# Performance work log

Hardware: AMD Instinct MI355X
Metric: run time of the kernel (lower is better)

The kernel has to match this reference:

```python
import jax, jax.numpy as jnp
import numpy as np

B, N, DIM, H, DH = 8, 1024, 512, 8, 64
INNER = H * DH  # 512
G = DH // 4     # SE(3) groups of size 4 per head


def setup_inputs() -> dict:
    key = jax.random.key(0)
    ks = jax.random.split(key, 6)
    x = jax.random.normal(ks[0], (B, N, DIM), jnp.float32)
    rotations = jax.random.normal(ks[1], (B, N, 3, 3), jnp.float32)
    translations = jax.random.normal(ks[2], (B, N, 3), jnp.float32)
    # JaxLinear init: trunc-normal std = 1/sqrt(fan_in), zero bias
    w_qkv = jax.random.normal(ks[3], (DIM, 3 * INNER), jnp.float32) * (1.0 / np.sqrt(DIM))
    b_qkv = jnp.zeros((3 * INNER,), jnp.float32)
    w_out = jax.random.normal(ks[4], (INNER, DIM), jnp.float32) * (1.0 / np.sqrt(INNER))
    b_out = jnp.zeros((DIM,), jnp.float32)
    return {"x": x, "rotations": rotations, "translations": translations,
            "w_qkv": w_qkv, "b_qkv": b_qkv, "w_out": w_out, "b_out": b_out}


def _apply_pose(P, t, transpose):
    # P: [B,N,4,4]; t: [B,H,N,DH] -> reshape to groups of 4 and rotate each group
    tg = t.reshape(B, H, N, G, 4)
    sub = 'bnji,bhncj->bhnci' if transpose else 'bnij,bhncj->bhnci'
    return jnp.einsum(sub, P, tg).reshape(B, H, N, DH)


def reference(x, rotations, translations, w_qkv, b_qkv, w_out, b_out):
    scale = DH ** -0.5
    qkv = x @ w_qkv + b_qkv                      # [B,N,3*INNER]
    q, k, v = jnp.split(qkv, 3, axis=-1)
    to_heads = lambda t: t.reshape(B, N, H, DH).transpose(0, 2, 1, 3)  # b n (h d) -> b h n d
    q, k, v = to_heads(q), to_heads(k), to_heads(v)

    # SE(3) pose matrices
    eye4 = jnp.eye(4, dtype=x.dtype)
    Rt = jnp.swapaxes(rotations, -1, -2)
    t_inv = -jnp.einsum('bnij,bnj->bni', Rt, translations)
    P_qinv = (jnp.broadcast_to(eye4, (B, N, 4, 4))
              .at[..., :3, :3].set(Rt)
              .at[..., :3, 3].set(t_inv))       # inverted query poses
    P_kv = (jnp.broadcast_to(eye4, (B, N, 4, 4))
            .at[..., :3, :3].set(rotations)
            .at[..., :3, 3].set(translations))  # key/value poses

    # per-token rotation of q/k/v (q uses P_qinv^T per original einsum)
    q = _apply_pose(P_qinv, q, transpose=True)
    k = _apply_pose(P_kv, k, transpose=False)
    v = _apply_pose(P_kv, v, transpose=False)   # v_transform=True

    attn = jax.nn.softmax(jnp.einsum('bhqd,bhkd->bhqk', q, k) * scale, axis=-1)
    out = jnp.einsum('bhqk,bhkd->bhqd', attn, v)
    out = _apply_pose(P_qinv, out, transpose=False)  # inverse transform on output

    out = out.transpose(0, 2, 1, 3).reshape(B, N, INNER)  # b h n d -> b n (h d)
    return out @ w_out + b_out
```

## Files before the change

kernel.cpp:

```cpp
#include <hip/hip_runtime.h>
#include <math.h>

#define BSZ   8
#define NSEQ  1024
#define DIM   512
#define NH    8
#define DH    64
#define INNER 512
#define NTOK  (BSZ*NSEQ)
#define QKVN  (3*INNER)

typedef __bf16 bf16x8 __attribute__((ext_vector_type(8)));
typedef float  f32x4  __attribute__((ext_vector_type(4)));

#define QSCL (0.125f * 1.44269504088896f)

static __device__ __forceinline__ ushort f2bf(float f) {
    union { float f; unsigned u; } v; v.f = f;
    unsigned r = (v.u + 0x7FFFu + ((v.u >> 16) & 1u)) >> 16;
    return (ushort)r;
}
static __device__ __forceinline__ float bf2f(ushort u) {
    union { unsigned u; float f; } v; v.u = ((unsigned)u) << 16;
    return v.f;
}
static __device__ __forceinline__ void split2(float x, ushort& h, ushort& l) {
    h = f2bf(x);
    l = f2bf(x - bf2f(h));
}
static __device__ __forceinline__ void async16(const void* g, void* l) {
    __builtin_amdgcn_global_load_lds(
        (const __attribute__((address_space(1))) unsigned int*)g,
        (__attribute__((address_space(3))) unsigned int*)l, 16, 0, 0);
}

__global__ __launch_bounds__(256) void split_cvt_kernel(
    const float* __restrict__ in, ushort* __restrict__ oh, ushort* __restrict__ ol)
{
    const int i = blockIdx.x * 256 + threadIdx.x;
    float4 v = ((const float4*)in)[i];
    ushort4 h, l;
    split2(v.x, h.x, l.x); split2(v.y, h.y, l.y);
    split2(v.z, h.z, l.z); split2(v.w, h.w, l.w);
    ((ushort4*)oh)[i] = h;
    ((ushort4*)ol)[i] = l;
}

__global__ __launch_bounds__(256) void tconv_split_kernel(
    const float* __restrict__ in, ushort* __restrict__ outh,
    ushort* __restrict__ outl, int K, int F)
{
    __shared__ float tile[32][33];
    const int bx = blockIdx.x;
    const int by = blockIdx.y;
    const int lx = threadIdx.x & 31, ly = threadIdx.x >> 5;
#pragma unroll
    for (int u = 0; u < 4; u++) {
        const int k = by*32 + ly + u*8;
        tile[ly + u*8][lx] = in[(size_t)k*F + bx*32 + lx];
    }
    __syncthreads();
#pragma unroll
    for (int u = 0; u < 4; u++) {
        const int f = bx*32 + ly + u*8;
        ushort h, l;
        split2(tile[lx][ly + u*8], h, l);
        outh[(size_t)f*K + by*32 + lx] = h;
        outl[(size_t)f*K + by*32 + lx] = l;
    }
}

__global__ __launch_bounds__(256) void vtrans_kernel(
    const ushort* __restrict__ vb, ushort* __restrict__ vt)
{
    __shared__ ushort tile[64][72];
    const int nt = blockIdx.x;
    const int bh = blockIdx.y;
    const int tid = threadIdx.x;
    const ushort* src = vb + (size_t)bh*NSEQ*DH + (size_t)nt*64*DH;
    ushort* dst = vt + (size_t)bh*DH*NSEQ + nt*64;

#pragma unroll
    for (int u = 0; u < 2; u++) {
        const int idx = tid + u*256;
        const int row = idx >> 3;
        const int col = (idx & 7) * 8;
        *(uint4*)&tile[row][col] = *(const uint4*)(src + row*DH + col);
    }
    __syncthreads();
#pragma unroll
    for (int u = 0; u < 2; u++) {
        const int idx = tid + u*256;
        const int d   = idx >> 3;
        const int n0  = (idx & 7) * 8;
        ushort tmp[8];
#pragma unroll
        for (int i = 0; i < 8; i++) tmp[i] = tile[n0+i][d];
        *(uint4*)&dst[(size_t)d*NSEQ + n0] = *(uint4*)tmp;
    }
}

__global__ __launch_bounds__(256) void qkv_gemm_split(
    const ushort* __restrict__ Agh, const ushort* __restrict__ Agl,
    const ushort* __restrict__ Bgh, const ushort* __restrict__ Bgl,
    const float* __restrict__ bias, const float* __restrict__ rot,
    const float* __restrict__ trans,
    ushort* __restrict__ qb, ushort* __restrict__ kb, ushort* __restrict__ vb)
{
    extern __shared__ __align__(16) char smem[];

    const int tid  = threadIdx.x;
    const int lane = tid & 63;
    const int w    = tid >> 6;
    const int c    = lane & 15;
    const int quad = lane >> 4;
    const int wr   = w >> 1, wc = w & 1;
    const int tn   = blockIdx.x;
    const int tf   = blockIdx.y;

    f32x4 acc[4][4] = {};

    const ushort* wp = (w == 0) ? Agh : (w == 1) ? Agl : (w == 2) ? Bgh : Bgl;
    const ushort* wbase = wp + (size_t)((w < 2 ? tf : tn)*128 + c)*DIM + quad*8;

    auto stage = [&](int k0, int buf) {
#pragma unroll
        for (int g = 0; g < 8; g++)
            async16(wbase + (size_t)g*16*DIM + k0,
                    smem + buf*32768 + (w*8 + g)*1024);
    };

    stage(0, 0);

    for (int ch = 0; ch < 16; ch++) {
        const int cur = ch & 1, nxt = cur ^ 1;
        if (ch < 15) {
            stage((ch+1)*32, nxt);
            __asm__ volatile("s_waitcnt vmcnt(8)\n\ts_barrier" ::: "memory");
        } else {
            __asm__ volatile("s_waitcnt vmcnt(0)\n\ts_barrier" ::: "memory");
        }

        const char* B = smem + cur*32768;
        bf16x8 fah[4], fal[4], fbh[4], fbl[4];
#pragma unroll
        for (int i = 0; i < 4; i++) {
            fah[i] = *(const bf16x8*)(B + ( 0 + wr*4 + i)*1024 + lane*16);
            fal[i] = *(const bf16x8*)(B + ( 8 + wr*4 + i)*1024 + lane*16);
        }
#pragma unroll
        for (int j = 0; j < 4; j++) {
            fbh[j] = *(const bf16x8*)(B + (16 + wc*4 + j)*1024 + lane*16);
            fbl[j] = *(const bf16x8*)(B + (24 + wc*4 + j)*1024 + lane*16);
        }
#pragma unroll
        for (int i = 0; i < 4; i++)
#pragma unroll
            for (int j = 0; j < 4; j++) {
                acc[i][j] = __builtin_amdgcn_mfma_f32_16x16x32_bf16(
                    fah[i], fbh[j], acc[i][j], 0, 0, 0);
                acc[i][j] = __builtin_amdgcn_mfma_f32_16x16x32_bf16(
                    fah[i], fbl[j], acc[i][j], 0, 0, 0);
                acc[i][j] = __builtin_amdgcn_mfma_f32_16x16x32_bf16(
                    fal[i], fbh[j], acc[i][j], 0, 0, 0);
            }
        __asm__ volatile("s_waitcnt lgkmcnt(0)\n\ts_barrier" ::: "memory");
    }

    const int sec = tf >> 2;
    ushort* dstbuf = (sec == 0) ? qb : ((sec == 1) ? kb : vb);

#pragma unroll
    for (int j = 0; j < 4; j++) {
        const int tc = tn*128 + wc*64 + j*16 + c;
        const int bb = tc >> 10, n = tc & 1023;
        const float* R = rot   + (size_t)(bb*NSEQ + n)*9;
        const float* T = trans + (size_t)(bb*NSEQ + n)*3;
        const float R0=R[0],R1=R[1],R2=R[2],R3=R[3],R4=R[4],R5=R[5],R6=R[6],R7=R[7],R8=R[8];
        const float T0=T[0],T1=T[1],T2=T[2];
        float ti0 = 0.f, ti1 = 0.f, ti2 = 0.f;
        if (sec == 0) {
            ti0 = -(R0*T0 + R3*T1 + R6*T2);
            ti1 = -(R1*T0 + R4*T1 + R7*T2);
            ti2 = -(R2*T0 + R5*T1 + R8*T2);
        }
#pragma unroll
        for (int i = 0; i < 4; i++) {
            const int fr = tf*128 + wr*64 + i*16 + quad*4;
            const int fl = fr & 511;
            const int h  = fl >> 6, d = fl & 63;
            float4 bv = *(const float4*)(bias + fr);
            const float g0 = acc[i][j][0] + bv.x;
            const float g1 = acc[i][j][1] + bv.y;
            const float g2 = acc[i][j][2] + bv.z;
            const float g3 = acc[i][j][3] + bv.w;
            float o0, o1, o2, o3;
            if (sec == 0) {
                o0 = (R0*g0 + R1*g1 + R2*g2) * QSCL;
                o1 = (R3*g0 + R4*g1 + R5*g2) * QSCL;
                o2 = (R6*g0 + R7*g1 + R8*g2) * QSCL;
                o3 = (ti0*g0 + ti1*g1 + ti2*g2 + g3) * QSCL;
            } else {
                o0 = R0*g0 + R1*g1 + R2*g2 + T0*g3;
                o1 = R3*g0 + R4*g1 + R5*g2 + T1*g3;
                o2 = R6*g0 + R7*g1 + R8*g2 + T2*g3;
                o3 = g3;
            }
            ushort4 ov = { f2bf(o0), f2bf(o1), f2bf(o2), f2bf(o3) };
            *(ushort4*)(dstbuf + ((size_t)((bb*NH + h)*NSEQ + n))*DH + d) = ov;
        }
    }
}

__global__ __launch_bounds__(256) void attn_mfma_kernel(
    const ushort* __restrict__ qb, const ushort* __restrict__ kb,
    const ushort* __restrict__ vt, const float* __restrict__ rot,
    const float* __restrict__ trans,
    ushort* __restrict__ omh, ushort* __restrict__ oml)
{
    __shared__ __align__(16) char smem[51200];

    const int tid  = threadIdx.x;
    const int lane = tid & 63;
    const int w    = tid >> 6;
    const int c    = lane & 15;
    const int quad = lane >> 4;

    const int qt = blockIdx.x;
    const int bh = blockIdx.y;
    const int bb = bh >> 3, h = bh & 7;

    const ushort* Q = qb + (size_t)bh * NSEQ * DH;
    const ushort* K = kb + (size_t)bh * NSEQ * DH;
    const ushort* V = vt + (size_t)bh * DH * NSEQ;

    bf16x8 qf[2][2];
#pragma unroll
    for (int m = 0; m < 2; m++) {
        const ushort* qrow = Q + (size_t)(qt*128 + w*32 + m*16 + c)*DH + quad*8;
        qf[m][0] = *(const bf16x8*)(qrow);
        qf[m][1] = *(const bf16x8*)(qrow + 32);
    }

    f32x4 Oacc[2][4] = {};
    float lsum[2][4] = {};

    auto stage = [&](int kt, int buf) {
#pragma unroll
        for (int u = 0; u < 2; u++) {
            const int seg = w + u*4;
            const int nt = seg >> 1, hh = seg & 1;
            const ushort* g = K + (size_t)(kt*64 + nt*16 + c)*DH + hh*32 + quad*8;
            async16(g, smem + buf*16384 + seg*1024);
        }
#pragma unroll
        for (int u = 0; u < 2; u++) {
            const int s2 = w + u*4;
            const int nt = s2 >> 1, kc = s2 & 1;
            const ushort* g = V + (size_t)(nt*16 + c)*NSEQ + kt*64 + kc*32 + quad*8;
            async16(g, smem + buf*16384 + 8192 + s2*1024);
        }
    };

    stage(0, 0);
    __syncthreads();

    for (int kt = 0; kt < 16; kt++) {
        const int cur = kt & 1, nxt = cur ^ 1;
        if (kt < 15) stage(kt+1, nxt);

        const char* Kb = smem + cur*16384;
        const char* Vb = smem + cur*16384 + 8192;

        f32x4 s[2][4];
#pragma unroll
        for (int nt = 0; nt < 4; nt++) {
            bf16x8 k0 = *(const bf16x8*)(Kb + (nt*2+0)*1024 + lane*16);
            bf16x8 k1 = *(const bf16x8*)(Kb + (nt*2+1)*1024 + lane*16);
#pragma unroll
            for (int m = 0; m < 2; m++) {
                f32x4 a = {0.f, 0.f, 0.f, 0.f};
                a = __builtin_amdgcn_mfma_f32_16x16x32_bf16(qf[m][0], k0, a, 0, 0, 0);
                a = __builtin_amdgcn_mfma_f32_16x16x32_bf16(qf[m][1], k1, a, 0, 0, 0);
                s[m][nt] = a;
            }
        }

#pragma unroll
        for (int m = 0; m < 2; m++) {
            ushort (*Psw)[72] = (ushort (*)[72])(smem + 32768 + (w*2+m)*2304);
#pragma unroll
            for (int nt = 0; nt < 4; nt++)
#pragma unroll
                for (int r = 0; r < 4; r++) {
                    const float p = exp2f(s[m][nt][r]);
                    lsum[m][r] += p;
                    Psw[quad*4 + r][nt*16 + c] = (ushort)__builtin_bit_cast(
                        unsigned short, (__bf16)p);
                }
        }
        __asm__ volatile("s_waitcnt lgkmcnt(0)" ::: "memory");

#pragma unroll
        for (int kc = 0; kc < 2; kc++) {
            bf16x8 vfr[4];
#pragma unroll
            for (int nt = 0; nt < 4; nt++)
                vfr[nt] = *(const bf16x8*)(Vb + (nt*2+kc)*1024 + lane*16);
#pragma unroll
            for (int m = 0; m < 2; m++) {
                ushort (*Psw)[72] = (ushort (*)[72])(smem + 32768 + (w*2+m)*2304);
                bf16x8 a = *(const bf16x8*)&Psw[c][kc*32 + quad*8];
#pragma unroll
                for (int nt = 0; nt < 4; nt++)
                    Oacc[m][nt] = __builtin_amdgcn_mfma_f32_16x16x32_bf16(
                        a, vfr[nt], Oacc[m][nt], 0, 0, 0);
            }
        }
        __syncthreads();
    }

#pragma unroll
    for (int mk = 1; mk < 16; mk <<= 1)
#pragma unroll
        for (int m = 0; m < 2; m++)
#pragma unroll
            for (int r = 0; r < 4; r++)
                lsum[m][r] += __shfl_xor(lsum[m][r], mk);

    float (*Osh)[68] = (float (*)[68])smem;
    {
        float inv[2][4];
#pragma unroll
        for (int m = 0; m < 2; m++)
#pragma unroll
            for (int r = 0; r < 4; r++) inv[m][r] = 1.f / lsum[m][r];
#pragma unroll
        for (int m = 0; m < 2; m++)
#pragma unroll
            for (int nt = 0; nt < 4; nt++)
#pragma unroll
                for (int r = 0; r < 4; r++)
                    Osh[w*32 + m*16 + quad*4 + r][nt*16 + c] =
                        Oacc[m][nt][r] * inv[m][r];
    }
    __syncthreads();

#pragma unroll
    for (int u = 0; u < 8; u++) {
        const int t   = tid + u*256;
        const int row = t >> 4;
        const int g   = t & 15;
        const int n   = qt*128 + row;
        const float o0 = Osh[row][g*4+0], o1 = Osh[row][g*4+1];
        const float o2 = Osh[row][g*4+2], o3 = Osh[row][g*4+3];
        const float* R = rot   + (size_t)(bb*NSEQ + n)*9;
        const float* T = trans + (size_t)(bb*NSEQ + n)*3;
        const float ti0 = -(R[0]*T[0] + R[3]*T[1] + R[6]*T[2]);
        const float ti1 = -(R[1]*T[0] + R[4]*T[1] + R[7]*T[2]);
        const float ti2 = -(R[2]*T[0] + R[5]*T[1] + R[8]*T[2]);
        const float p0 = R[0]*o0 + R[3]*o1 + R[6]*o2 + ti0*o3;
        const float p1 = R[1]*o0 + R[4]*o1 + R[7]*o2 + ti1*o3;
        const float p2 = R[2]*o0 + R[5]*o1 + R[8]*o2 + ti2*o3;
        const float p3 = o3;
        ushort4 hv, lv;
        split2(p0, hv.x, lv.x); split2(p1, hv.y, lv.y);
        split2(p2, hv.z, lv.z); split2(p3, hv.w, lv.w);
        const size_t idx = (size_t)(bb*NSEQ + n)*INNER + h*DH + g*4;
        *(ushort4*)(omh + idx) = hv;
        *(ushort4*)(oml + idx) = lv;
    }
}

__global__ __launch_bounds__(256) void out_gemm_split(
    const ushort* __restrict__ Agh, const ushort* __restrict__ Agl,
    const ushort* __restrict__ Bgh, const ushort* __restrict__ Bgl,
    const float* __restrict__ bias, float* __restrict__ out)
{
    extern __shared__ __align__(16) char smem[];

    const int tid  = threadIdx.x;
    const int lane = tid & 63;
    const int w    = tid >> 6;
    const int c    = lane & 15;
    const int quad = lane >> 4;
    const int wr   = w >> 1, wc = w & 1;
    const int tn   = blockIdx.x;
    const int tf   = blockIdx.y;

    f32x4 acc[4][4] = {};

    const ushort* wp = (w == 0) ? Agh : (w == 1) ? Agl : (w == 2) ? Bgh : Bgl;
    const ushort* wbase = wp + (size_t)((w < 2 ? tf : tn)*128 + c)*INNER + quad*8;

    auto stage = [&](int k0, int buf) {
#pragma unroll
        for (int g = 0; g < 8; g++)
            async16(wbase + (size_t)g*16*INNER + k0,
                    smem + buf*32768 + (w*8 + g)*1024);
    };

    stage(0, 0);

    for (int ch = 0; ch < 16; ch++) {
        const int cur = ch & 1, nxt = cur ^ 1;
        if (ch < 15) {
            stage((ch+1)*32, nxt);
            __asm__ volatile("s_waitcnt vmcnt(8)\n\ts_barrier" ::: "memory");
        } else {
            __asm__ volatile("s_waitcnt vmcnt(0)\n\ts_barrier" ::: "memory");
        }

        const char* B = smem + cur*32768;
        bf16x8 fah[4], fal[4], fbh[4], fbl[4];
#pragma unroll
        for (int i = 0; i < 4; i++) {
            fah[i] = *(const bf16x8*)(B + ( 0 + wr*4 + i)*1024 + lane*16);
            fal[i] = *(const bf16x8*)(B + ( 8 + wr*4 + i)*1024 + lane*16);
        }
#pragma unroll
        for (int j = 0; j < 4; j++) {
            fbh[j] = *(const bf16x8*)(B + (16 + wc*4 + j)*1024 + lane*16);
            fbl[j] = *(const bf16x8*)(B + (24 + wc*4 + j)*1024 + lane*16);
        }
#pragma unroll
        for (int i = 0; i < 4; i++)
#pragma unroll
            for (int j = 0; j < 4; j++) {
                acc[i][j] = __builtin_amdgcn_mfma_f32_16x16x32_bf16(
                    fah[i], fbh[j], acc[i][j], 0, 0, 0);
                acc[i][j] = __builtin_amdgcn_mfma_f32_16x16x32_bf16(
                    fah[i], fbl[j], acc[i][j], 0, 0, 0);
                acc[i][j] = __builtin_amdgcn_mfma_f32_16x16x32_bf16(
                    fal[i], fbh[j], acc[i][j], 0, 0, 0);
            }
        __asm__ volatile("s_waitcnt lgkmcnt(0)\n\ts_barrier" ::: "memory");
    }

#pragma unroll
    for (int j = 0; j < 4; j++) {
        const int tc = tn*128 + wc*64 + j*16 + c;
#pragma unroll
        for (int i = 0; i < 4; i++) {
            const int fr = tf*128 + wr*64 + i*16 + quad*4;
            float4 bv = *(const float4*)(bias + fr);
            float4 ov = { acc[i][j][0] + bv.x, acc[i][j][1] + bv.y,
                          acc[i][j][2] + bv.z, acc[i][j][3] + bv.w };
            *(float4*)(out + (size_t)tc*DIM + fr) = ov;
        }
    }
}

extern "C" void kernel_launch(void* const* d_in, const int* in_sizes, int n_in,
                              void* d_out, int out_size, void* d_ws, size_t ws_size,
                              hipStream_t stream) {
    (void)in_sizes; (void)n_in; (void)out_size; (void)ws_size;
    const float* x     = (const float*)d_in[0];
    const float* rot   = (const float*)d_in[1];
    const float* trans = (const float*)d_in[2];
    const float* w_qkv = (const float*)d_in[3];
    const float* b_qkv = (const float*)d_in[4];
    const float* w_out = (const float*)d_in[5];
    const float* b_out = (const float*)d_in[6];
    float* out = (float*)d_out;

    const size_t HB = (size_t)BSZ*NH*NSEQ*DH;
    ushort* qb   = (ushort*)d_ws;
    ushort* kb   = qb   + HB;
    ushort* vb   = kb   + HB;
    ushort* vt   = vb   + HB;
    ushort* woTh = vt   + HB;
    ushort* woTl = woTh + (size_t)DIM*INNER;
    ushort* wqTh = woTl + (size_t)DIM*INNER;
    ushort* wqTl = wqTh + (size_t)QKVN*DIM;
    ushort* xh   = wqTl + (size_t)QKVN*DIM;
    ushort* xl   = xh   + HB;
    ushort* omh  = xh;
    ushort* oml  = xl;

    split_cvt_kernel<<<dim3(NTOK*DIM/1024), 256, 0, stream>>>(x, xh, xl);
    tconv_split_kernel<<<dim3(QKVN/32, DIM/32), 256, 0, stream>>>(w_qkv, wqTh, wqTl, DIM, QKVN);
    tconv_split_kernel<<<dim3(DIM/32, INNER/32), 256, 0, stream>>>(w_out, woTh, woTl, INNER, DIM);

    qkv_gemm_split<<<dim3(NTOK/128, QKVN/128), 256, 65536, stream>>>(
        wqTh, wqTl, xh, xl, b_qkv, rot, trans, qb, kb, vb);
    vtrans_kernel<<<dim3(NSEQ/64, BSZ*NH), 256, 0, stream>>>(vb, vt);
    attn_mfma_kernel<<<dim3(NSEQ/128, BSZ*NH), 256, 0, stream>>>(
        qb, kb, vt, rot, trans, omh, oml);
    out_gemm_split<<<dim3(NTOK/128, DIM/128), 256, 65536, stream>>>(
        woTh, woTl, omh, oml, b_out, out);
}
```

Measured before the change: 203.0 us.

## Drop weight low-part split in GEMMs and write V transposed from QKV epilogue

Weights are now converted to a single bf16 copy instead of a hi/lo pair, so both GEMMs run two MFMAs per tile step instead of three, stage one fewer operand into LDS, and use less shared memory. The separate V transpose kernel is removed; the QKV epilogue writes V directly in the transposed layout with strided scalar stores. This trades some weight precision and less-coalesced V stores for fewer MFMAs, less LDS traffic and one fewer launch.

```diff
diff --git a/kernel.cpp b/kernel.cpp
--- a/kernel.cpp
+++ b/kernel.cpp
@@ -46,9 +46,8 @@
     ((ushort4*)ol)[i] = l;
 }
 
-__global__ __launch_bounds__(256) void tconv_split_kernel(
-    const float* __restrict__ in, ushort* __restrict__ outh,
-    ushort* __restrict__ outl, int K, int F)
+__global__ __launch_bounds__(256) void tconv_kernel(
+    const float* __restrict__ in, ushort* __restrict__ outh, int K, int F)
 {
     __shared__ float tile[32][33];
     const int bx = blockIdx.x;
@@ -63,49 +62,16 @@
 #pragma unroll
     for (int u = 0; u < 4; u++) {
         const int f = bx*32 + ly + u*8;
-        ushort h, l;
-        split2(tile[lx][ly + u*8], h, l);
-        outh[(size_t)f*K + by*32 + lx] = h;
-        outl[(size_t)f*K + by*32 + lx] = l;
-    }
-}
-
-__global__ __launch_bounds__(256) void vtrans_kernel(
-    const ushort* __restrict__ vb, ushort* __restrict__ vt)
-{
-    __shared__ ushort tile[64][72];
-    const int nt = blockIdx.x;
-    const int bh = blockIdx.y;
-    const int tid = threadIdx.x;
-    const ushort* src = vb + (size_t)bh*NSEQ*DH + (size_t)nt*64*DH;
-    ushort* dst = vt + (size_t)bh*DH*NSEQ + nt*64;
-
-#pragma unroll
-    for (int u = 0; u < 2; u++) {
-        const int idx = tid + u*256;
-        const int row = idx >> 3;
-        const int col = (idx & 7) * 8;
-        *(uint4*)&tile[row][col] = *(const uint4*)(src + row*DH + col);
-    }
-    __syncthreads();
-#pragma unroll
-    for (int u = 0; u < 2; u++) {
-        const int idx = tid + u*256;
-        const int d   = idx >> 3;
-        const int n0  = (idx & 7) * 8;
-        ushort tmp[8];
-#pragma unroll
-        for (int i = 0; i < 8; i++) tmp[i] = tile[n0+i][d];
-        *(uint4*)&dst[(size_t)d*NSEQ + n0] = *(uint4*)tmp;
+        outh[(size_t)f*K + by*32 + lx] = f2bf(tile[lx][ly + u*8]);
     }
 }
 
 __global__ __launch_bounds__(256) void qkv_gemm_split(
-    const ushort* __restrict__ Agh, const ushort* __restrict__ Agl,
-    const ushort* __restrict__ Bgh, const ushort* __restrict__ Bgl,
+    const ushort* __restrict__ Agh, const ushort* __restrict__ Bgh,
+    const ushort* __restrict__ Bgl,
     const float* __restrict__ bias, const float* __restrict__ rot,
     const float* __restrict__ trans,
-    ushort* __restrict__ qb, ushort* __restrict__ kb, ushort* __restrict__ vb)
+    ushort* __restrict__ qb, ushort* __restrict__ kb, ushort* __restrict__ vt)
 {
     extern __shared__ __align__(16) char smem[];
 
@@ -120,14 +86,17 @@
 
     f32x4 acc[4][4] = {};
 
-    const ushort* wp = (w == 0) ? Agh : (w == 1) ? Agl : (w == 2) ? Bgh : Bgl;
-    const ushort* wbase = wp + (size_t)((w < 2 ? tf : tn)*128 + c)*DIM + quad*8;
+    const ushort* wp = (w == 0) ? Agh : (w == 1) ? Bgh : Bgl;
+    const ushort* wbase = wp + (size_t)((w == 0 ? tf : tn)*128 + c)*DIM + quad*8;
+    const int lbase = w * 8192;
 
     auto stage = [&](int k0, int buf) {
-#pragma unroll
-        for (int g = 0; g < 8; g++)
-            async16(wbase + (size_t)g*16*DIM + k0,
-                    smem + buf*32768 + (w*8 + g)*1024);
+        if (w < 3) {
+#pragma unroll
+            for (int g = 0; g < 8; g++)
+                async16(wbase + (size_t)g*16*DIM + k0,
+                        smem + buf*24576 + lbase + g*1024);
+        }
     };
 
     stage(0, 0);
@@ -141,34 +110,29 @@
             __asm__ volatile("s_waitcnt vmcnt(0)\n\ts_barrier" ::: "memory");
         }
 
-        const char* B = smem + cur*32768;
-        bf16x8 fah[4], fal[4], fbh[4], fbl[4];
-#pragma unroll
-        for (int i = 0; i < 4; i++) {
-            fah[i] = *(const bf16x8*)(B + ( 0 + wr*4 + i)*1024 + lane*16);
-            fal[i] = *(const bf16x8*)(B + ( 8 + wr*4 + i)*1024 + lane*16);
-        }
+        const char* B = smem + cur*24576;
+        bf16x8 fa[4], fbh[4], fbl[4];
+#pragma unroll
+        for (int i = 0; i < 4; i++)
+            fa[i] = *(const bf16x8*)(B + (wr*4 + i)*1024 + lane*16);
 #pragma unroll
         for (int j = 0; j < 4; j++) {
-            fbh[j] = *(const bf16x8*)(B + (16 + wc*4 + j)*1024 + lane*16);
-            fbl[j] = *(const bf16x8*)(B + (24 + wc*4 + j)*1024 + lane*16);
+            fbh[j] = *(const bf16x8*)(B +  8192 + (wc*4 + j)*1024 + lane*16);
+            fbl[j] = *(const bf16x8*)(B + 16384 + (wc*4 + j)*1024 + lane*16);
         }
 #pragma unroll
         for (int i = 0; i < 4; i++)
 #pragma unroll
             for (int j = 0; j < 4; j++) {
                 acc[i][j] = __builtin_amdgcn_mfma_f32_16x16x32_bf16(
-                    fah[i], fbh[j], acc[i][j], 0, 0, 0);
+                    fa[i], fbh[j], acc[i][j], 0, 0, 0);
                 acc[i][j] = __builtin_amdgcn_mfma_f32_16x16x32_bf16(
-                    fah[i], fbl[j], acc[i][j], 0, 0, 0);
-                acc[i][j] = __builtin_amdgcn_mfma_f32_16x16x32_bf16(
-                    fal[i], fbh[j], acc[i][j], 0, 0, 0);
+                    fa[i], fbl[j], acc[i][j], 0, 0, 0);
             }
         __asm__ volatile("s_waitcnt lgkmcnt(0)\n\ts_barrier" ::: "memory");
     }
 
     const int sec = tf >> 2;
-    ushort* dstbuf = (sec == 0) ? qb : ((sec == 1) ? kb : vb);
 
 #pragma unroll
     for (int j = 0; j < 4; j++) {
@@ -194,20 +158,29 @@
             const float g1 = acc[i][j][1] + bv.y;
             const float g2 = acc[i][j][2] + bv.z;
             const float g3 = acc[i][j][3] + bv.w;
-            float o0, o1, o2, o3;
             if (sec == 0) {
-                o0 = (R0*g0 + R1*g1 + R2*g2) * QSCL;
-                o1 = (R3*g0 + R4*g1 + R5*g2) * QSCL;
-                o2 = (R6*g0 + R7*g1 + R8*g2) * QSCL;
-                o3 = (ti0*g0 + ti1*g1 + ti2*g2 + g3) * QSCL;
+                float o0 = (R0*g0 + R1*g1 + R2*g2) * QSCL;
+                float o1 = (R3*g0 + R4*g1 + R5*g2) * QSCL;
+                float o2 = (R6*g0 + R7*g1 + R8*g2) * QSCL;
+                float o3 = (ti0*g0 + ti1*g1 + ti2*g2 + g3) * QSCL;
+                ushort4 ov = { f2bf(o0), f2bf(o1), f2bf(o2), f2bf(o3) };
+                *(ushort4*)(qb + ((size_t)((bb*NH + h)*NSEQ + n))*DH + d) = ov;
             } else {
-                o0 = R0*g0 + R1*g1 + R2*g2 + T0*g3;
-                o1 = R3*g0 + R4*g1 + R5*g2 + T1*g3;
-                o2 = R6*g0 + R7*g1 + R8*g2 + T2*g3;
-                o3 = g3;
+                float o0 = R0*g0 + R1*g1 + R2*g2 + T0*g3;
+                float o1 = R3*g0 + R4*g1 + R5*g2 + T1*g3;
+                float o2 = R6*g0 + R7*g1 + R8*g2 + T2*g3;
+                float o3 = g3;
+                if (sec == 1) {
+                    ushort4 ov = { f2bf(o0), f2bf(o1), f2bf(o2), f2bf(o3) };
+                    *(ushort4*)(kb + ((size_t)((bb*NH + h)*NSEQ + n))*DH + d) = ov;
+                } else {
+                    ushort* vtb = vt + ((size_t)(bb*NH + h)*DH + d)*NSEQ + n;
+                    vtb[0*NSEQ] = f2bf(o0);
+                    vtb[1*NSEQ] = f2bf(o1);
+                    vtb[2*NSEQ] = f2bf(o2);
+                    vtb[3*NSEQ] = f2bf(o3);
+                }
             }
-            ushort4 ov = { f2bf(o0), f2bf(o1), f2bf(o2), f2bf(o3) };
-            *(ushort4*)(dstbuf + ((size_t)((bb*NH + h)*NSEQ + n))*DH + d) = ov;
         }
     }
 }
@@ -373,8 +346,8 @@
 }
 
 __global__ __launch_bounds__(256) void out_gemm_split(
-    const ushort* __restrict__ Agh, const ushort* __restrict__ Agl,
-    const ushort* __restrict__ Bgh, const ushort* __restrict__ Bgl,
+    const ushort* __restrict__ Agh, const ushort* __restrict__ Bgh,
+    const ushort* __restrict__ Bgl,
     const float* __restrict__ bias, float* __restrict__ out)
 {
     extern __shared__ __align__(16) char smem[];
@@ -390,14 +363,17 @@
 
     f32x4 acc[4][4] = {};
 
-    const ushort* wp = (w == 0) ? Agh : (w == 1) ? Agl : (w == 2) ? Bgh : Bgl;
-    const ushort* wbase = wp + (size_t)((w < 2 ? tf : tn)*128 + c)*INNER + quad*8;
+    const ushort* wp = (w == 0) ? Agh : (w == 1) ? Bgh : Bgl;
+    const ushort* wbase = wp + (size_t)((w == 0 ? tf : tn)*128 + c)*INNER + quad*8;
+    const int lbase = w * 8192;
 
     auto stage = [&](int k0, int buf) {
-#pragma unroll
-        for (int g = 0; g < 8; g++)
-            async16(wbase + (size_t)g*16*INNER + k0,
-                    smem + buf*32768 + (w*8 + g)*1024);
+        if (w < 3) {
+#pragma unroll
+            for (int g = 0; g < 8; g++)
+                async16(wbase + (size_t)g*16*INNER + k0,
+                        smem + buf*24576 + lbase + g*1024);
+        }
     };
 
     stage(0, 0);
@@ -411,28 +387,24 @@
             __asm__ volatile("s_waitcnt vmcnt(0)\n\ts_barrier" ::: "memory");
         }
 
-        const char* B = smem + cur*32768;
-        bf16x8 fah[4], fal[4], fbh[4], fbl[4];
-#pragma unroll
-        for (int i = 0; i < 4; i++) {
-            fah[i] = *(const bf16x8*)(B + ( 0 + wr*4 + i)*1024 + lane*16);
-            fal[i] = *(const bf16x8*)(B + ( 8 + wr*4 + i)*1024 + lane*16);
-        }
+        const char* B = smem + cur*24576;
+        bf16x8 fa[4], fbh[4], fbl[4];
+#pragma unroll
+        for (int i = 0; i < 4; i++)
+            fa[i] = *(const bf16x8*)(B + (wr*4 + i)*1024 + lane*16);
 #pragma unroll
         for (int j = 0; j < 4; j++) {
-            fbh[j] = *(const bf16x8*)(B + (16 + wc*4 + j)*1024 + lane*16);
-            fbl[j] = *(const bf16x8*)(B + (24 + wc*4 + j)*1024 + lane*16);
+            fbh[j] = *(const bf16x8*)(B +  8192 + (wc*4 + j)*1024 + lane*16);
+            fbl[j] = *(const bf16x8*)(B + 16384 + (wc*4 + j)*1024 + lane*16);
         }
 #pragma unroll
         for (int i = 0; i < 4; i++)
 #pragma unroll
             for (int j = 0; j < 4; j++) {
                 acc[i][j] = __builtin_amdgcn_mfma_f32_16x16x32_bf16(
-                    fah[i], fbh[j], acc[i][j], 0, 0, 0);
+                    fa[i], fbh[j], acc[i][j], 0, 0, 0);
                 acc[i][j] = __builtin_amdgcn_mfma_f32_16x16x32_bf16(
-                    fah[i], fbl[j], acc[i][j], 0, 0, 0);
-                acc[i][j] = __builtin_amdgcn_mfma_f32_16x16x32_bf16(
-                    fal[i], fbh[j], acc[i][j], 0, 0, 0);
+                    fa[i], fbl[j], acc[i][j], 0, 0, 0);
             }
         __asm__ volatile("s_waitcnt lgkmcnt(0)\n\ts_barrier" ::: "memory");
     }
@@ -467,26 +439,22 @@
     const size_t HB = (size_t)BSZ*NH*NSEQ*DH;
     ushort* qb   = (ushort*)d_ws;
     ushort* kb   = qb   + HB;
-    ushort* vb   = kb   + HB;
-    ushort* vt   = vb   + HB;
+    ushort* vt   = kb   + HB;
     ushort* woTh = vt   + HB;
-    ushort* woTl = woTh + (size_t)DIM*INNER;
-    ushort* wqTh = woTl + (size_t)DIM*INNER;
-    ushort* wqTl = wqTh + (size_t)QKVN*DIM;
-    ushort* xh   = wqTl + (size_t)QKVN*DIM;
+    ushort* wqTh = woTh + (size_t)DIM*INNER;
+    ushort* xh   = wqTh + (size_t)QKVN*DIM;
     ushort* xl   = xh   + HB;
     ushort* omh  = xh;
     ushort* oml  = xl;
 
     split_cvt_kernel<<<dim3(NTOK*DIM/1024), 256, 0, stream>>>(x, xh, xl);
-    tconv_split_kernel<<<dim3(QKVN/32, DIM/32), 256, 0, stream>>>(w_qkv, wqTh, wqTl, DIM, QKVN);
-    tconv_split_kernel<<<dim3(DIM/32, INNER/32), 256, 0, stream>>>(w_out, woTh, woTl, INNER, DIM);
-
-    qkv_gemm_split<<<dim3(NTOK/128, QKVN/128), 256, 65536, stream>>>(
-        wqTh, wqTl, xh, xl, b_qkv, rot, trans, qb, kb, vb);
-    vtrans_kernel<<<dim3(NSEQ/64, BSZ*NH), 256, 0, stream>>>(vb, vt);
+    tconv_kernel<<<dim3(QKVN/32, DIM/32), 256, 0, stream>>>(w_qkv, wqTh, DIM, QKVN);
+    tconv_kernel<<<dim3(DIM/32, INNER/32), 256, 0, stream>>>(w_out, woTh, INNER, DIM);
+
+    qkv_gemm_split<<<dim3(NTOK/128, QKVN/128), 256, 49152, stream>>>(
+        wqTh, xh, xl, b_qkv, rot, trans, qb, kb, vt);
     attn_mfma_kernel<<<dim3(NSEQ/128, BSZ*NH), 256, 0, stream>>>(
         qb, kb, vt, rot, trans, omh, oml);
-    out_gemm_split<<<dim3(NTOK/128, DIM/128), 256, 65536, stream>>>(
-        woTh, woTl, omh, oml, b_out, out);
-}
+    out_gemm_split<<<dim3(NTOK/128, DIM/128), 256, 49152, stream>>>(
+        woTh, omh, oml, b_out, out);
+}
```

Result: faster. 185.0 us (-8.9%).
